# Optimization experiments

Measured on AMD Instinct MI355X. Metric: run time of the kernel, lower is better.

The kernel has to match this reference:

```python
import jax, jax.numpy as jnp
import numpy as np

LEN_SORT_WINDOW = 2


def _butterfly_indices(v_len, d_v):
    # Column j is arange rolled right by s_j: s_0 = s_1 = 0, s_j = 2*(j-1) mod v_len.
    # (The butterfly_factor_to_matrix result in the original code is discarded;
    #  only the cyclic shifts matter.)
    shifts = np.zeros(d_v, dtype=np.int64)
    if d_v > 1:
        shifts[1:] = (LEN_SORT_WINDOW * np.arange(d_v - 1, dtype=np.int64)) % v_len
    rows = np.arange(v_len, dtype=np.int64)[:, None]
    return jnp.asarray((rows - shifts[None, :]) % v_len)  # [v_len, d_v] int64


def setup_inputs() -> dict:
    key = jax.random.key(0)
    B, L, D = 8, 4096, 1024
    v = jax.random.normal(key, (B, L, D), dtype=jnp.float32)
    return {"v": v}


def reference(v) -> jnp.ndarray:
    B, L, D = v.shape
    idx = _butterfly_indices(L, D)                       # [L, D]
    # gather: v_shifted[b,i,j] = v[b, idx[i,j], j]
    v_shifted = jnp.take_along_axis(v, jnp.broadcast_to(idx[None], (B, L, D)), axis=1)
    # windowed pairwise sort (ascending, window = 2) along the sequence dim
    pairs = v_shifted.reshape(B, L // LEN_SORT_WINDOW, LEN_SORT_WINDOW, D)
    v_sorted = jnp.sort(pairs, axis=2)
    return v_sorted.reshape(B, L, D)
```

## Files before the change

kernel.cpp:

```cpp
#include <hip/hip_runtime.h>

namespace {

constexpr int B  = 8;
constexpr int L  = 4096;
constexpr int D  = 1024;
constexpr int P  = L / 2;
constexpr int TJ = 32;
constexpr int TP = 128;
constexpr int RTOT = TP + TJ;
constexpr int NT = 256;

__global__ __launch_bounds__(NT)
void swd_kernel(const float* __restrict__ v, float* __restrict__ out) {
  const int j0 = blockIdx.x * TJ;
  const int p0 = blockIdx.y * TP;
  const int b  = blockIdx.z;

  __shared__ float lds_m[RTOT][TJ];
  __shared__ float lds_M[RTOT][TJ];

  const int hmax = j0 + TJ - 2;
  const int r0   = p0 - hmax;

  const float* __restrict__ vb = v + (size_t)b * L * D + j0;

  for (int idx = threadIdx.x; idx < RTOT * TJ; idx += NT) {
    const int k  = idx / TJ;
    const int jj = idx - k * TJ;
    const int q  = (r0 + k) & (P - 1);
    const size_t base = (size_t)(2 * q) * D + jj;
    const float a0 = vb[base];
    const float a1 = vb[base + D];
    lds_m[k][jj] = fminf(a0, a1);
    lds_M[k][jj] = fmaxf(a0, a1);
  }
  __syncthreads();

  float* __restrict__ ob = out + (size_t)b * L * D + j0;
  for (int idx = threadIdx.x; idx < TP * TJ; idx += NT) {
    const int pp = idx / TJ;
    const int jj = idx - pp * TJ;
    const int j  = j0 + jj;
    const int h  = (j == 0) ? 0 : (j - 1);
    const int k  = pp + (hmax - h);
    const size_t o = (size_t)(2 * (p0 + pp)) * D + jj;
    ob[o]     = lds_m[k][jj];
    ob[o + D] = lds_M[k][jj];
  }
}

}

extern "C" void kernel_launch(void* const* d_in, const int* , int ,
                              void* d_out, int , void* , size_t ,
                              hipStream_t stream) {
  const float* v = (const float*)d_in[0];
  float* out = (float*)d_out;
  dim3 grid(D / TJ, P / TP, B);
  swd_kernel<<<grid, NT, 0, stream>>>(v, out);
}
```

Measured before the change: 240.8 us.

## Vectorize loads and stores with float4 and gather skewed output from padded LDS

Global loads and stores now use float4 instead of scalar floats. The output phase is restructured so each thread writes two pairs of rows for a 4-column group, picking each lane from the appropriately shifted LDS row. The LDS rows are padded to 36 floats, and the thread count is doubled to 512 so that each thread handles exactly one output group. The aim is fewer memory instructions and wider transactions on a bandwidth-bound gather. The trade-off is more intricate index logic, including a special case for column 0.

```diff
diff --git a/kernel.cpp b/kernel.cpp
--- a/kernel.cpp
+++ b/kernel.cpp
@@ -5,49 +5,75 @@
 constexpr int B  = 8;
 constexpr int L  = 4096;
 constexpr int D  = 1024;
+constexpr int D4 = D / 4;
 constexpr int P  = L / 2;
 constexpr int TJ = 32;
+constexpr int G  = TJ / 4;
 constexpr int TP = 128;
 constexpr int RTOT = TP + TJ;
-constexpr int NT = 256;
+constexpr int LDW  = TJ + 4;
+constexpr int NT = 512;
 
 __global__ __launch_bounds__(NT)
-void swd_kernel(const float* __restrict__ v, float* __restrict__ out) {
+void swd_kernel(const float4* __restrict__ v, float4* __restrict__ out) {
   const int j0 = blockIdx.x * TJ;
   const int p0 = blockIdx.y * TP;
   const int b  = blockIdx.z;
 
-  __shared__ float lds_m[RTOT][TJ];
-  __shared__ float lds_M[RTOT][TJ];
+  __shared__ __align__(16) float lds_m[RTOT][LDW];
+  __shared__ __align__(16) float lds_M[RTOT][LDW];
 
   const int hmax = j0 + TJ - 2;
   const int r0   = p0 - hmax;
 
-  const float* __restrict__ vb = v + (size_t)b * L * D + j0;
+  const float4* __restrict__ vb = v + (size_t)b * L * D4 + (j0 >> 2);
 
-  for (int idx = threadIdx.x; idx < RTOT * TJ; idx += NT) {
-    const int k  = idx / TJ;
-    const int jj = idx - k * TJ;
+  for (int idx = threadIdx.x; idx < RTOT * G; idx += NT) {
+    const int k  = idx >> 3;
+    const int fg = idx & 7;
     const int q  = (r0 + k) & (P - 1);
-    const size_t base = (size_t)(2 * q) * D + jj;
-    const float a0 = vb[base];
-    const float a1 = vb[base + D];
-    lds_m[k][jj] = fminf(a0, a1);
-    lds_M[k][jj] = fmaxf(a0, a1);
+    const float4 a0 = vb[(size_t)(2 * q) * D4 + fg];
+    const float4 a1 = vb[(size_t)(2 * q + 1) * D4 + fg];
+    float4 m, M;
+    m.x = fminf(a0.x, a1.x); M.x = fmaxf(a0.x, a1.x);
+    m.y = fminf(a0.y, a1.y); M.y = fmaxf(a0.y, a1.y);
+    m.z = fminf(a0.z, a1.z); M.z = fmaxf(a0.z, a1.z);
+    m.w = fminf(a0.w, a1.w); M.w = fmaxf(a0.w, a1.w);
+    *(float4*)&lds_m[k][4 * fg] = m;
+    *(float4*)&lds_M[k][4 * fg] = M;
   }
   __syncthreads();
 
-  float* __restrict__ ob = out + (size_t)b * L * D + j0;
-  for (int idx = threadIdx.x; idx < TP * TJ; idx += NT) {
-    const int pp = idx / TJ;
-    const int jj = idx - pp * TJ;
-    const int j  = j0 + jj;
-    const int h  = (j == 0) ? 0 : (j - 1);
-    const int k  = pp + (hmax - h);
-    const size_t o = (size_t)(2 * (p0 + pp)) * D + jj;
-    ob[o]     = lds_m[k][jj];
-    ob[o + D] = lds_M[k][jj];
-  }
+  const int g   = threadIdx.x & 7;
+  const int c   = threadIdx.x >> 3;
+  const int pp0 = c * 2;
+  const int kx = pp0 + (TJ - 1) - 4 * g;
+
+  const float4 m0 = *(const float4*)&lds_m[kx - 3][4 * g];
+  const float4 m1 = *(const float4*)&lds_m[kx - 2][4 * g];
+  const float4 m2 = *(const float4*)&lds_m[kx - 1][4 * g];
+  const float4 m3 = *(const float4*)&lds_m[kx    ][4 * g];
+  const float4 m4 = *(const float4*)&lds_m[kx + 1][4 * g];
+  const float4 M0 = *(const float4*)&lds_M[kx - 3][4 * g];
+  const float4 M1 = *(const float4*)&lds_M[kx - 2][4 * g];
+  const float4 M2 = *(const float4*)&lds_M[kx - 1][4 * g];
+  const float4 M3 = *(const float4*)&lds_M[kx    ][4 * g];
+  const float4 M4 = *(const float4*)&lds_M[kx + 1][4 * g];
+
+  const bool sp = (j0 == 0) && (g == 0);
+
+  float4 e0, o0, e1, o1;
+  e0.x = sp ? m2.x : m3.x; e0.y = m2.y; e0.z = m1.z; e0.w = m0.w;
+  o0.x = sp ? M2.x : M3.x; o0.y = M2.y; o0.z = M1.z; o0.w = M0.w;
+  e1.x = sp ? m3.x : m4.x; e1.y = m3.y; e1.z = m2.z; e1.w = m1.w;
+  o1.x = sp ? M3.x : M4.x; o1.y = M3.y; o1.z = M2.z; o1.w = M1.w;
+
+  float4* __restrict__ ob = out + (size_t)b * L * D4 + (j0 >> 2) + g;
+  const size_t ro = (size_t)(2 * (p0 + pp0)) * D4;
+  ob[ro]            = e0;
+  ob[ro + D4]       = o0;
+  ob[ro + 2 * D4]   = e1;
+  ob[ro + 3 * D4]   = o1;
 }
 
 }
@@ -55,8 +81,8 @@
 extern "C" void kernel_launch(void* const* d_in, const int* , int ,
                               void* d_out, int , void* , size_t ,
                               hipStream_t stream) {
-  const float* v = (const float*)d_in[0];
-  float* out = (float*)d_out;
+  const float4* v = (const float4*)d_in[0];
+  float4* out = (float4*)d_out;
   dim3 grid(D / TJ, P / TP, B);
   swd_kernel<<<grid, NT, 0, stream>>>(v, out);
 }
```

Result: faster. 233.9 us (-2.9%).
